# Performance work log

Hardware: AMD Instinct MI355X
Metric: run time of the kernel (lower is better)

The kernel has to match this reference:

```python
import jax, jax.numpy as jnp
import numpy as np

EPS = 1e-5

def _layernorm(x, g, b):
    mu = jnp.mean(x, axis=-1, keepdims=True)
    var = jnp.mean(jnp.square(x - mu), axis=-1, keepdims=True)
    return (x - mu) * jax.lax.rsqrt(var + EPS) * g + b

def setup_inputs() -> dict:
    key = jax.random.key(0)
    ks = jax.random.split(key, 5)
    dims, head = 1024, 16
    b, n = 2, 2048
    s = 0.02
    return {
        "x": jax.random.normal(ks[0], (b, n, dims), dtype=jnp.float32),
        "ln_g": jnp.ones((dims,), dtype=jnp.float32),
        "ln_b": jnp.zeros((dims,), dtype=jnp.float32),
        "W_kv": jax.random.normal(ks[1], (dims, 2 * dims), dtype=jnp.float32) * s,
        "W_x": jax.random.normal(ks[2], (head, head), dtype=jnp.float32) * s,
        "W_xa": jax.random.normal(ks[3], (head, head), dtype=jnp.float32) * s,
        "W_out": jax.random.normal(ks[4], (dims, dims), dtype=jnp.float32) * s,
    }

def reference(x, ln_g, ln_b, W_kv, W_x, W_xa, W_out):
    # attentiond.forward with xa=None, mask=None (self.que / self.rope are unused in the original forward)
    b, n, dims = x.shape
    head = W_x.shape[0]
    hd = dims // head
    h = _layernorm(x, ln_g, ln_b)
    kv = h @ W_kv                               # [b, n, 2*dims]
    qk, v = jnp.split(kv, 2, axis=-1)
    # xa is None -> qka = qk, va = v
    qk = qk.reshape(b, n, head, hd).transpose(0, 2, 1, 3)   # [b, h, n, d]
    v = v.reshape(b, n, head, hd).transpose(0, 2, 1, 3)
    scores = jnp.einsum('bhqd,bhkd->bhqk', qk, qk)          # full score matrix (no 1/sqrt(d) scale in original)
    a1 = jax.nn.softmax(scores, axis=-1)
    a2 = jax.nn.softmax(scores, axis=-2)
    # 1x1 Conv2d over head channel = head-mixing matmul: out[g] = sum_h W[g,h] * in[h]
    a1 = jnp.einsum('gh,bhqk->bgqk', W_x, a1)
    a2 = jnp.einsum('gh,bhqk->bgqk', W_xa, a2)
    o1 = jnp.einsum('bhij,bhjd->bhid', a1, v)               # used path (va == v)
    _o2 = jnp.einsum('bhji,bhjd->bhid', a2, v)              # computed in original but discarded (dead code)
    o1 = o1.transpose(0, 2, 1, 3).reshape(b, n, dims)
    return o1 @ W_out
```

## Files before the change

### kernel.cpp

```cpp
#include <hip/hip_runtime.h>
#include <math.h>

constexpr int Bb   = 2;
constexpr int Nn   = 2048;
constexpr int Dd   = 1024;
constexpr int Hh   = 16;
constexpr int HD   = 64;
constexpr int KVW  = 2*Dd;
constexpr int KSL  = 512;
constexpr float SHIFT = 20.f;

typedef short bf16x8 __attribute__((ext_vector_type(8)));
typedef float f32x4  __attribute__((ext_vector_type(4)));

__device__ inline float bf2f(unsigned short u){
  union { unsigned int i; float f; } x; x.i = ((unsigned int)u) << 16; return x.f;
}
__device__ inline unsigned short f2bf(float f){
  union { float f; unsigned int i; } x; x.f = f;
  unsigned int r = x.i + 0x7fffu + ((x.i >> 16) & 1u);
  return (unsigned short)(r >> 16);
}
__device__ inline void storeC(float* p, float v, int accum){ if (accum) *p += v; else *p = v; }
__device__ inline void storeC(unsigned short* p, float v, int){ *p = f2bf(v); }

__global__ __launch_bounds__(256) void ln_kernel(const float* __restrict__ x,
    const float* __restrict__ g, const float* __restrict__ bta, unsigned short* __restrict__ h){
  int row = blockIdx.x, tid = threadIdx.x;
  const float4* x4 = (const float4*)(x + (size_t)row*Dd);
  float4 v = x4[tid];
  float s  = v.x+v.y+v.z+v.w;
  float s2 = v.x*v.x+v.y*v.y+v.z*v.z+v.w*v.w;
#pragma unroll
  for (int off=32; off>0; off>>=1){ s += __shfl_down(s,off); s2 += __shfl_down(s2,off); }
  __shared__ float red[8];
  if ((tid&63)==0){ red[tid>>6]=s; red[4+(tid>>6)]=s2; }
  __syncthreads();
  s  = red[0]+red[1]+red[2]+red[3];
  s2 = red[4]+red[5]+red[6]+red[7];
  float mu = s*(1.f/Dd);
  float rs = rsqrtf(fmaxf(s2*(1.f/Dd)-mu*mu,0.f)+1e-5f);
  float4 gv=((const float4*)g)[tid], bv=((const float4*)bta)[tid];
  ushort4 o;
  o.x=f2bf((v.x-mu)*rs*gv.x+bv.x); o.y=f2bf((v.y-mu)*rs*gv.y+bv.y);
  o.z=f2bf((v.z-mu)*rs*gv.z+bv.z); o.w=f2bf((v.w-mu)*rs*gv.w+bv.w);
  ((ushort4*)(h+(size_t)row*Dd))[tid]=o;
}

__global__ __launch_bounds__(256) void wT_kernel(const float* __restrict__ in,
    unsigned short* __restrict__ out, int R, int Cc){
  __shared__ float t[32][33];
  int c0 = blockIdx.x*32, r0 = blockIdx.y*32;
  int tx = threadIdx.x&31, ty = threadIdx.x>>5;
#pragma unroll
  for (int k=0;k<4;k++)
    t[ty+8*k][tx] = in[(size_t)(r0+ty+8*k)*Cc + c0+tx];
  __syncthreads();
#pragma unroll
  for (int k=0;k<4;k++)
    out[(size_t)(c0+ty+8*k)*R + r0+tx] = f2bf(t[tx][ty+8*k]);
}

__global__ __launch_bounds__(256) void vT_kernel(const unsigned short* __restrict__ kvb,
    unsigned short* __restrict__ vT){
  __shared__ unsigned short t[32][33];
  int b = blockIdx.z;
  int d0 = blockIdx.x*32, k0 = blockIdx.y*32;
  const unsigned short* in = kvb + (size_t)b*Nn*KVW + Dd;
  unsigned short* out = vT + (size_t)b*Dd*Nn;
  int tx = threadIdx.x&31, ty = threadIdx.x>>5;
#pragma unroll
  for (int k=0;k<4;k++)
    t[ty+8*k][tx] = in[(size_t)(k0+ty+8*k)*KVW + d0+tx];
  __syncthreads();
#pragma unroll
  for (int k=0;k<4;k++)
    out[(size_t)(d0+ty+8*k)*Nn + k0+tx] = t[tx][ty+8*k];
}

__global__ __launch_bounds__(256) void cvt_kernel(const float* __restrict__ in,
    unsigned short* __restrict__ out){
  int i = blockIdx.x*256 + threadIdx.x;
  float4 v = ((const float4*)in)[i];
  ushort4 o; o.x=f2bf(v.x); o.y=f2bf(v.y); o.z=f2bf(v.z); o.w=f2bf(v.w);
  ((ushort4*)out)[i] = o;
}

__global__ __launch_bounds__(256) void zero_kernel(float* __restrict__ p){
  ((float4*)p)[blockIdx.x*256 + threadIdx.x] = float4{0.f,0.f,0.f,0.f};
}

template <int BN, typename CT>
__global__ __launch_bounds__(256) void mgemm(
    const unsigned short* __restrict__ A, const unsigned short* __restrict__ Bt,
    CT* __restrict__ C, int K, int lda, int ldb, int ldc,
    long sAz, long sBz, long sCz, int accum){
  constexpr int BM = 128, BK = 32;
  constexpr int RS = 40;
  constexpr int WC = (BN==128)?2:1;
  constexpr int WR = 4/WC;
  constexpr int FM = BM/(WR*16);
  constexpr int FN = BN/(WC*16);
  __shared__ __align__(16) short As[BM*RS];
  __shared__ __align__(16) short Bs[BN*RS];
  int tid = threadIdx.x;
  long z = blockIdx.z;
  const unsigned short* Ab = A + z*sAz + (size_t)blockIdx.y*BM*lda;
  const unsigned short* Bb = Bt + z*sBz + (size_t)blockIdx.x*BN*ldb;
  CT* Cb = C + z*sCz + (size_t)blockIdx.y*BM*ldc + (size_t)blockIdx.x*BN;
  int wid = tid>>6, lane = tid&63;
  int wr = (WC==2)?(wid>>1):wid;
  int wc = (WC==2)?(wid&1):0;
  int r0 = tid>>2, s0 = tid&3;
  f32x4 acc[FM][FN] = {};
  int nk = K/BK;
  uint4 a0, a1, b0, b1;
  a0 = *(const uint4*)(Ab + (size_t)r0*lda + s0*8);
  a1 = *(const uint4*)(Ab + (size_t)(r0+64)*lda + s0*8);
  b0 = *(const uint4*)(Bb + (size_t)r0*ldb + s0*8);
  if constexpr (BN==128) b1 = *(const uint4*)(Bb + (size_t)(r0+64)*ldb + s0*8);
  *(uint4*)&As[r0*RS + s0*8]      = a0;
  *(uint4*)&As[(r0+64)*RS + s0*8] = a1;
  *(uint4*)&Bs[r0*RS + s0*8]      = b0;
  if constexpr (BN==128) *(uint4*)&Bs[(r0+64)*RS + s0*8] = b1;
  __syncthreads();
  for (int t=0; t<nk; t++){
    if (t+1 < nk){
      int k0 = (t+1)*BK;
      a0 = *(const uint4*)(Ab + (size_t)r0*lda + k0 + s0*8);
      a1 = *(const uint4*)(Ab + (size_t)(r0+64)*lda + k0 + s0*8);
      b0 = *(const uint4*)(Bb + (size_t)r0*ldb + k0 + s0*8);
      if constexpr (BN==128) b1 = *(const uint4*)(Bb + (size_t)(r0+64)*ldb + k0 + s0*8);
    }
    bf16x8 af[FM], bfr[FN];
#pragma unroll
    for (int m=0;m<FM;m++){
      int row = wr*(FM*16) + m*16 + (lane&15);
      af[m] = *(const bf16x8*)&As[row*RS + (lane>>4)*8];
    }
#pragma unroll
    for (int n=0;n<FN;n++){
      int col = wc*(FN*16) + n*16 + (lane&15);
      bfr[n] = *(const bf16x8*)&Bs[col*RS + (lane>>4)*8];
    }
#pragma unroll
    for (int m=0;m<FM;m++)
#pragma unroll
      for (int n=0;n<FN;n++)
        acc[m][n] = __builtin_amdgcn_mfma_f32_16x16x32_bf16(af[m], bfr[n], acc[m][n], 0, 0, 0);
    if (t+1 < nk){
      __syncthreads();
      *(uint4*)&As[r0*RS + s0*8]      = a0;
      *(uint4*)&As[(r0+64)*RS + s0*8] = a1;
      *(uint4*)&Bs[r0*RS + s0*8]      = b0;
      if constexpr (BN==128) *(uint4*)&Bs[(r0+64)*RS + s0*8] = b1;
      __syncthreads();
    }
  }
#pragma unroll
  for (int m=0;m<FM;m++){
    int row = wr*(FM*16) + m*16 + (lane>>4)*4;
#pragma unroll
    for (int n=0;n<FN;n++){
      int col = wc*(FN*16) + n*16 + (lane&15);
#pragma unroll
      for (int rg=0;rg<4;rg++)
        storeC(Cb + (size_t)(row+rg)*ldc + col, acc[m][n][rg], accum);
    }
  }
}

__global__ __launch_bounds__(256) void sqexp_kernel(
    const unsigned short* __restrict__ A,
    const unsigned short* __restrict__ Bt,
    unsigned short* __restrict__ U,
    float* __restrict__ lsum){
  constexpr int BM = 128, BN = 128, BK = 32, RS = 40;
  constexpr int FM = 4, FN = 4;
  __shared__ __align__(16) short As[BM*RS];
  __shared__ __align__(16) short Bs[BN*RS];
  int tid = threadIdx.x;
  long z = blockIdx.z;
  const unsigned short* Ab = A + z*HD + (size_t)blockIdx.y*BM*KVW;
  const unsigned short* Bb = Bt + z*HD + (size_t)blockIdx.x*BN*KVW;
  unsigned short* Ub = U + z*(size_t)Nn*Nn + (size_t)blockIdx.y*BM*Nn + (size_t)blockIdx.x*BN;
  float* lrow = lsum + z*Nn + blockIdx.y*BM;
  int wid = tid>>6, lane = tid&63;
  int wr = wid>>1, wc = wid&1;
  int r0 = tid>>2, s0 = tid&3;
  f32x4 acc[FM][FN] = {};
  uint4 a0, a1, b0, b1;
  a0 = *(const uint4*)(Ab + (size_t)r0*KVW + s0*8);
  a1 = *(const uint4*)(Ab + (size_t)(r0+64)*KVW + s0*8);
  b0 = *(const uint4*)(Bb + (size_t)r0*KVW + s0*8);
  b1 = *(const uint4*)(Bb + (size_t)(r0+64)*KVW + s0*8);
  *(uint4*)&As[r0*RS + s0*8]      = a0;
  *(uint4*)&As[(r0+64)*RS + s0*8] = a1;
  *(uint4*)&Bs[r0*RS + s0*8]      = b0;
  *(uint4*)&Bs[(r0+64)*RS + s0*8] = b1;
  __syncthreads();
  for (int t=0; t<HD/BK; t++){
    if (t == 0){
      a0 = *(const uint4*)(Ab + (size_t)r0*KVW + BK + s0*8);
      a1 = *(const uint4*)(Ab + (size_t)(r0+64)*KVW + BK + s0*8);
      b0 = *(const uint4*)(Bb + (size_t)r0*KVW + BK + s0*8);
      b1 = *(const uint4*)(Bb + (size_t)(r0+64)*KVW + BK + s0*8);
    }
    bf16x8 af[FM], bfr[FN];
#pragma unroll
    for (int m=0;m<FM;m++)
      af[m] = *(const bf16x8*)&As[(wr*64 + m*16 + (lane&15))*RS + (lane>>4)*8];
#pragma unroll
    for (int n=0;n<FN;n++)
      bfr[n] = *(const bf16x8*)&Bs[(wc*64 + n*16 + (lane&15))*RS + (lane>>4)*8];
#pragma unroll
    for (int m=0;m<FM;m++)
#pragma unroll
      for (int n=0;n<FN;n++)
        acc[m][n] = __builtin_amdgcn_mfma_f32_16x16x32_bf16(af[m], bfr[n], acc[m][n], 0, 0, 0);
    if (t == 0){
      __syncthreads();
      *(uint4*)&As[r0*RS + s0*8]      = a0;
      *(uint4*)&As[(r0+64)*RS + s0*8] = a1;
      *(uint4*)&Bs[r0*RS + s0*8]      = b0;
      *(uint4*)&Bs[(r0+64)*RS + s0*8] = b1;
      __syncthreads();
    }
  }
  float part[FM][4];
#pragma unroll
  for (int m=0;m<FM;m++)
#pragma unroll
    for (int rg=0;rg<4;rg++) part[m][rg] = 0.f;
#pragma unroll
  for (int m=0;m<FM;m++){
    int row = wr*64 + m*16 + (lane>>4)*4;
#pragma unroll
    for (int n=0;n<FN;n++){
      int col = wc*64 + n*16 + (lane&15);
#pragma unroll
      for (int rg=0;rg<4;rg++){
        float e = __expf(acc[m][n][rg] - SHIFT);
        Ub[(size_t)(row+rg)*Nn + col] = f2bf(e);
        part[m][rg] += e;
      }
    }
  }
#pragma unroll
  for (int m=0;m<FM;m++)
#pragma unroll
    for (int rg=0;rg<4;rg++){
      float s = part[m][rg];
#pragma unroll
      for (int off=1; off<16; off<<=1) s += __shfl_xor(s, off);
      if ((lane&15)==0)
        atomicAdd(&lrow[wr*64 + m*16 + (lane>>4)*4 + rg], s);
    }
}

__global__ __launch_bounds__(256) void mix2s_kernel(
    const unsigned short* __restrict__ U, const float* __restrict__ Wx,
    const float* __restrict__ lsum, unsigned short* __restrict__ PM, int k0){
  int tid = threadIdx.x;
  int qr = tid>>7;
  int q  = blockIdx.x*2 + qr;
  int kk = (tid&127)*4;
  __shared__ float Wl[256];
  __shared__ float rl[2][16];
  Wl[tid] = Wx[tid];
  if (tid < 32) rl[tid>>4][tid&15] = 1.f/lsum[(size_t)(tid&15)*Nn + blockIdx.x*2 + (tid>>4)];
  __syncthreads();
  int ks = k0 + kk;
  float pm[16][4] = {};
#pragma unroll
  for (int h=0;h<16;h++){
    ushort4 u4 = *(const ushort4*)&U[((size_t)h*Nn+q)*Nn + ks];
    float r = rl[qr][h];
    float f0=bf2f(u4.x)*r, f1=bf2f(u4.y)*r, f2=bf2f(u4.z)*r, f3=bf2f(u4.w)*r;
#pragma unroll
    for (int g=0;g<16;g++){
      float w = Wl[g*16+h];
      pm[g][0]+=w*f0; pm[g][1]+=w*f1; pm[g][2]+=w*f2; pm[g][3]+=w*f3;
    }
  }
#pragma unroll
  for (int g=0;g<16;g++){
    ushort4 o;
    o.x=f2bf(pm[g][0]); o.y=f2bf(pm[g][1]); o.z=f2bf(pm[g][2]); o.w=f2bf(pm[g][3]);
    *(ushort4*)&PM[((size_t)g*Nn+q)*KSL + kk] = o;
  }
}

extern "C" void kernel_launch(void* const* d_in, const int* in_sizes, int n_in,
                              void* d_out, int out_size, void* d_ws, size_t ws_size,
                              hipStream_t stream){
  (void)in_sizes; (void)n_in; (void)out_size; (void)ws_size;
  const float* x    = (const float*)d_in[0];
  const float* lng  = (const float*)d_in[1];
  const float* lnb  = (const float*)d_in[2];
  const float* Wkv  = (const float*)d_in[3];
  const float* Wx   = (const float*)d_in[4];
  const float* Wout = (const float*)d_in[6];
  float* out = (float*)d_out;

  char* p = (char*)d_ws;
  unsigned short* h_b   = (unsigned short*)p;
  float*          o1    = (float*)p;
  p += (size_t)Bb*Nn*Dd*2;
  unsigned short* kvb   = (unsigned short*)p; p += (size_t)Bb*Nn*KVW*2;
  unsigned short* WkvT  = (unsigned short*)p; p += (size_t)KVW*Dd*2;
  unsigned short* WoutT = (unsigned short*)p; p += (size_t)Dd*Dd*2;
  unsigned short* vTb   = (unsigned short*)p; p += (size_t)Bb*Dd*Nn*2;
  unsigned short* o1b   = (unsigned short*)p; p += (size_t)Bb*Nn*Dd*2;
  float*          lb    = (float*)p;          p += (size_t)Bb*Hh*Nn*4;
  unsigned short* U     = (unsigned short*)p; p += (size_t)Hh*Nn*Nn*2;
  unsigned short* PM    = (unsigned short*)p;

  wT_kernel<<<dim3(KVW/32, Dd/32), 256, 0, stream>>>(Wkv, WkvT, Dd, KVW);
  wT_kernel<<<dim3(Dd/32, Dd/32), 256, 0, stream>>>(Wout, WoutT, Dd, Dd);
  ln_kernel<<<Bb*Nn, 256, 0, stream>>>(x, lng, lnb, h_b);
  mgemm<128, unsigned short><<<dim3(KVW/128, (Bb*Nn)/128, 1), 256, 0, stream>>>(
      h_b, WkvT, kvb, Dd, Dd, Dd, KVW, 0, 0, 0, 0);
  vT_kernel<<<dim3(Dd/32, Nn/32, Bb), 256, 0, stream>>>(kvb, vTb);
  zero_kernel<<<(Bb*Hh*Nn)/1024, 256, 0, stream>>>(lb);

  for (int b=0;b<Bb;b++){
    const unsigned short* kvb_b = kvb + (size_t)b*Nn*KVW;
    float* lb_b = lb + (size_t)b*Hh*Nn;
    sqexp_kernel<<<dim3(Nn/128, Nn/128, Hh), 256, 0, stream>>>(kvb_b, kvb_b, U, lb_b);
    for (int k0=0;k0<Nn;k0+=KSL){
      mix2s_kernel<<<Nn/2, 256, 0, stream>>>(U, Wx, lb_b, PM, k0);
      mgemm<64, float><<<dim3(1, Nn/128, Hh), 256, 0, stream>>>(
          PM, vTb + (size_t)b*Dd*Nn + k0, o1,
          KSL, KSL, Nn, Dd, (long)Nn*KSL, (long)64*Nn, 64, k0>0);
    }
    cvt_kernel<<<(Nn*Dd)/1024, 256, 0, stream>>>(o1, o1b + (size_t)b*Nn*Dd);
  }
  mgemm<128, float><<<dim3(Dd/128, (Bb*Nn)/128, 1), 256, 0, stream>>>(
      o1b, WoutT, out, Dd, Dd, Dd, Dd, 0, 0, 0, 0);
}
```

Before: 490.0 us.

## Recompute QK^T scores in fused exp-mix kernel instead of storing U

The old path wrote the exponentiated score tensor U to memory in bf16 and read it back in the mixing kernel. That path is replaced by a stats-only pass that computes row sums, plus a fused kernel that recomputes QK^T with MFMA, exponentiates, normalizes and mixes heads before writing PM. The K-slice loop, the float accumulation buffer and the conversion kernel are gone: the PV GEMM now runs over full K and writes bf16 output directly. The trade-off is computing the score GEMM twice to save a large write and read of the score tensor, with a full-size PM buffer in place of slices.

New measurement: 408.7 us. 16.6% less time.

```diff
diff --git a/kernel.cpp b/kernel.cpp
--- a/kernel.cpp
+++ b/kernel.cpp
@@ -7,7 +7,6 @@
 constexpr int Hh   = 16;
 constexpr int HD   = 64;
 constexpr int KVW  = 2*Dd;
-constexpr int KSL  = 512;
 constexpr float SHIFT = 20.f;
 
 typedef short bf16x8 __attribute__((ext_vector_type(8)));
@@ -76,14 +75,6 @@
 #pragma unroll
   for (int k=0;k<4;k++)
     out[(size_t)(d0+ty+8*k)*Nn + k0+tx] = t[tx][ty+8*k];
-}
-
-__global__ __launch_bounds__(256) void cvt_kernel(const float* __restrict__ in,
-    unsigned short* __restrict__ out){
-  int i = blockIdx.x*256 + threadIdx.x;
-  float4 v = ((const float4*)in)[i];
-  ushort4 o; o.x=f2bf(v.x); o.y=f2bf(v.y); o.z=f2bf(v.z); o.w=f2bf(v.w);
-  ((ushort4*)out)[i] = o;
 }
 
 __global__ __launch_bounds__(256) void zero_kernel(float* __restrict__ p){
@@ -170,21 +161,19 @@
   }
 }
 
-__global__ __launch_bounds__(256) void sqexp_kernel(
-    const unsigned short* __restrict__ A,
-    const unsigned short* __restrict__ Bt,
-    unsigned short* __restrict__ U,
+__global__ __launch_bounds__(256) void statsl_kernel(
+    const unsigned short* __restrict__ kvb,
     float* __restrict__ lsum){
-  constexpr int BM = 128, BN = 128, BK = 32, RS = 40;
+  constexpr int BK = 32, RS = 40;
   constexpr int FM = 4, FN = 4;
-  __shared__ __align__(16) short As[BM*RS];
-  __shared__ __align__(16) short Bs[BN*RS];
+  __shared__ __align__(16) short As[128*RS];
+  __shared__ __align__(16) short Bs[128*RS];
   int tid = threadIdx.x;
-  long z = blockIdx.z;
-  const unsigned short* Ab = A + z*HD + (size_t)blockIdx.y*BM*KVW;
-  const unsigned short* Bb = Bt + z*HD + (size_t)blockIdx.x*BN*KVW;
-  unsigned short* Ub = U + z*(size_t)Nn*Nn + (size_t)blockIdx.y*BM*Nn + (size_t)blockIdx.x*BN;
-  float* lrow = lsum + z*Nn + blockIdx.y*BM;
+  int z = blockIdx.z;
+  const unsigned short* base = kvb + (size_t)(z>>4)*Nn*KVW + (z&15)*HD;
+  const unsigned short* Ab = base + (size_t)blockIdx.y*128*KVW;
+  const unsigned short* Bq = base + (size_t)blockIdx.x*128*KVW;
+  float* lrow = lsum + (size_t)z*Nn + blockIdx.y*128;
   int wid = tid>>6, lane = tid&63;
   int wr = wid>>1, wc = wid&1;
   int r0 = tid>>2, s0 = tid&3;
@@ -192,8 +181,8 @@
   uint4 a0, a1, b0, b1;
   a0 = *(const uint4*)(Ab + (size_t)r0*KVW + s0*8);
   a1 = *(const uint4*)(Ab + (size_t)(r0+64)*KVW + s0*8);
-  b0 = *(const uint4*)(Bb + (size_t)r0*KVW + s0*8);
-  b1 = *(const uint4*)(Bb + (size_t)(r0+64)*KVW + s0*8);
+  b0 = *(const uint4*)(Bq + (size_t)r0*KVW + s0*8);
+  b1 = *(const uint4*)(Bq + (size_t)(r0+64)*KVW + s0*8);
   *(uint4*)&As[r0*RS + s0*8]      = a0;
   *(uint4*)&As[(r0+64)*RS + s0*8] = a1;
   *(uint4*)&Bs[r0*RS + s0*8]      = b0;
@@ -203,8 +192,8 @@
     if (t == 0){
       a0 = *(const uint4*)(Ab + (size_t)r0*KVW + BK + s0*8);
       a1 = *(const uint4*)(Ab + (size_t)(r0+64)*KVW + BK + s0*8);
-      b0 = *(const uint4*)(Bb + (size_t)r0*KVW + BK + s0*8);
-      b1 = *(const uint4*)(Bb + (size_t)(r0+64)*KVW + BK + s0*8);
+      b0 = *(const uint4*)(Bq + (size_t)r0*KVW + BK + s0*8);
+      b1 = *(const uint4*)(Bq + (size_t)(r0+64)*KVW + BK + s0*8);
     }
     bf16x8 af[FM], bfr[FN];
 #pragma unroll
@@ -233,19 +222,12 @@
 #pragma unroll
     for (int rg=0;rg<4;rg++) part[m][rg] = 0.f;
 #pragma unroll
-  for (int m=0;m<FM;m++){
-    int row = wr*64 + m*16 + (lane>>4)*4;
-#pragma unroll
-    for (int n=0;n<FN;n++){
-      int col = wc*64 + n*16 + (lane&15);
-#pragma unroll
-      for (int rg=0;rg<4;rg++){
-        float e = __expf(acc[m][n][rg] - SHIFT);
-        Ub[(size_t)(row+rg)*Nn + col] = f2bf(e);
-        part[m][rg] += e;
-      }
-    }
-  }
+  for (int m=0;m<FM;m++)
+#pragma unroll
+    for (int n=0;n<FN;n++)
+#pragma unroll
+      for (int rg=0;rg<4;rg++)
+        part[m][rg] += __expf(acc[m][n][rg] - SHIFT);
 #pragma unroll
   for (int m=0;m<FM;m++)
 #pragma unroll
@@ -258,36 +240,77 @@
     }
 }
 
-__global__ __launch_bounds__(256) void mix2s_kernel(
-    const unsigned short* __restrict__ U, const float* __restrict__ Wx,
-    const float* __restrict__ lsum, unsigned short* __restrict__ PM, int k0){
+__global__ __launch_bounds__(256) void mixexp_kernel(
+    const unsigned short* __restrict__ kvb_b,
+    const float* __restrict__ Wx,
+    const float* __restrict__ lsum_b,
+    unsigned short* __restrict__ PM){
+  constexpr int QS = 72;
+  __shared__ __align__(16) short Qs[16*QS];
+  __shared__ __align__(16) short Ks[64*QS];
+  __shared__ float Wl[256];
+  __shared__ float rls[16][16];
   int tid = threadIdx.x;
-  int qr = tid>>7;
-  int q  = blockIdx.x*2 + qr;
-  int kk = (tid&127)*4;
-  __shared__ float Wl[256];
-  __shared__ float rl[2][16];
+  int k0 = blockIdx.x*64, q0 = blockIdx.y*16;
+  int wv = tid>>6, lane = tid&63;
   Wl[tid] = Wx[tid];
-  if (tid < 32) rl[tid>>4][tid&15] = 1.f/lsum[(size_t)(tid&15)*Nn + blockIdx.x*2 + (tid>>4)];
-  __syncthreads();
-  int ks = k0 + kk;
-  float pm[16][4] = {};
-#pragma unroll
-  for (int h=0;h<16;h++){
-    ushort4 u4 = *(const ushort4*)&U[((size_t)h*Nn+q)*Nn + ks];
-    float r = rl[qr][h];
-    float f0=bf2f(u4.x)*r, f1=bf2f(u4.y)*r, f2=bf2f(u4.z)*r, f3=bf2f(u4.w)*r;
-#pragma unroll
-    for (int g=0;g<16;g++){
-      float w = Wl[g*16+h];
-      pm[g][0]+=w*f0; pm[g][1]+=w*f1; pm[g][2]+=w*f2; pm[g][3]+=w*f3;
-    }
-  }
-#pragma unroll
-  for (int g=0;g<16;g++){
-    ushort4 o;
-    o.x=f2bf(pm[g][0]); o.y=f2bf(pm[g][1]); o.z=f2bf(pm[g][2]); o.w=f2bf(pm[g][3]);
-    *(ushort4*)&PM[((size_t)g*Nn+q)*KSL + kk] = o;
+  {
+    int h = tid>>4, r = tid&15;
+    rls[h][r] = 1.f/lsum_b[(size_t)h*Nn + q0 + r];
+  }
+  int qr = tid>>4, qc = (tid&15)*4;
+  int kr = tid>>2, kc = (tid&3)*16;
+  const unsigned short* Qg = kvb_b + (size_t)(q0+qr)*KVW + qc;
+  const unsigned short* Kg = kvb_b + (size_t)(k0+kr)*KVW + kc;
+  uint2 qv; uint4 kv0, kv1;
+  qv  = *(const uint2*)(Qg);
+  kv0 = *(const uint4*)(Kg);
+  kv1 = *(const uint4*)(Kg + 8);
+  *(uint2*)&Qs[qr*QS + qc]     = qv;
+  *(uint4*)&Ks[kr*QS + kc]     = kv0;
+  *(uint4*)&Ks[kr*QS + kc + 8] = kv1;
+  __syncthreads();
+  float pmacc[16][4] = {};
+  for (int h=0; h<16; h++){
+    if (h+1 < 16){
+      qv  = *(const uint2*)(Qg + (h+1)*64);
+      kv0 = *(const uint4*)(Kg + (h+1)*64);
+      kv1 = *(const uint4*)(Kg + (h+1)*64 + 8);
+    }
+    bf16x8 af0 = *(const bf16x8*)&Qs[(lane&15)*QS + (lane>>4)*8];
+    bf16x8 af1 = *(const bf16x8*)&Qs[(lane&15)*QS + (lane>>4)*8 + 32];
+    bf16x8 bf0 = *(const bf16x8*)&Ks[(wv*16+(lane&15))*QS + (lane>>4)*8];
+    bf16x8 bf1 = *(const bf16x8*)&Ks[(wv*16+(lane&15))*QS + (lane>>4)*8 + 32];
+    f32x4 acc = {};
+    acc = __builtin_amdgcn_mfma_f32_16x16x32_bf16(af0, bf0, acc, 0, 0, 0);
+    acc = __builtin_amdgcn_mfma_f32_16x16x32_bf16(af1, bf1, acc, 0, 0, 0);
+    float er[4];
+#pragma unroll
+    for (int rg=0; rg<4; rg++)
+      er[rg] = __expf(acc[rg] - SHIFT) * rls[h][(lane>>4)*4 + rg];
+#pragma unroll
+    for (int g=0; g<16; g++){
+      float w = Wl[g*16 + h];
+#pragma unroll
+      for (int rg=0; rg<4; rg++) pmacc[g][rg] += w*er[rg];
+    }
+    if (h+1 < 16){
+      __syncthreads();
+      *(uint2*)&Qs[qr*QS + qc]     = qv;
+      *(uint4*)&Ks[kr*QS + kc]     = kv0;
+      *(uint4*)&Ks[kr*QS + kc + 8] = kv1;
+      __syncthreads();
+    }
+  }
+  int col = k0 + wv*16 + (lane&15);
+#pragma unroll
+  for (int g=0; g<16; g++){
+    unsigned short* Pg = PM + ((size_t)g*Nn + q0)*Nn + col;
+#pragma unroll
+    for (int rg=0; rg<4; rg++){
+      int row = (lane>>4)*4 + rg;
+      Pg[(size_t)row*Nn] = f2bf(pmacc[g][rg]);
+    }
   }
 }
 
@@ -304,16 +327,13 @@
   float* out = (float*)d_out;
 
   char* p = (char*)d_ws;
-  unsigned short* h_b   = (unsigned short*)p;
-  float*          o1    = (float*)p;
-  p += (size_t)Bb*Nn*Dd*2;
+  unsigned short* h_b   = (unsigned short*)p; p += (size_t)Bb*Nn*Dd*2;
   unsigned short* kvb   = (unsigned short*)p; p += (size_t)Bb*Nn*KVW*2;
   unsigned short* WkvT  = (unsigned short*)p; p += (size_t)KVW*Dd*2;
   unsigned short* WoutT = (unsigned short*)p; p += (size_t)Dd*Dd*2;
   unsigned short* vTb   = (unsigned short*)p; p += (size_t)Bb*Dd*Nn*2;
   unsigned short* o1b   = (unsigned short*)p; p += (size_t)Bb*Nn*Dd*2;
   float*          lb    = (float*)p;          p += (size_t)Bb*Hh*Nn*4;
-  unsigned short* U     = (unsigned short*)p; p += (size_t)Hh*Nn*Nn*2;
   unsigned short* PM    = (unsigned short*)p;
 
   wT_kernel<<<dim3(KVW/32, Dd/32), 256, 0, stream>>>(Wkv, WkvT, Dd, KVW);
@@ -324,17 +344,15 @@
   vT_kernel<<<dim3(Dd/32, Nn/32, Bb), 256, 0, stream>>>(kvb, vTb);
   zero_kernel<<<(Bb*Hh*Nn)/1024, 256, 0, stream>>>(lb);
 
+  statsl_kernel<<<dim3(Nn/128, Nn/128, Bb*Hh), 256, 0, stream>>>(kvb, lb);
+
   for (int b=0;b<Bb;b++){
     const unsigned short* kvb_b = kvb + (size_t)b*Nn*KVW;
-    float* lb_b = lb + (size_t)b*Hh*Nn;
-    sqexp_kernel<<<dim3(Nn/128, Nn/128, Hh), 256, 0, stream>>>(kvb_b, kvb_b, U, lb_b);
-    for (int k0=0;k0<Nn;k0+=KSL){
-      mix2s_kernel<<<Nn/2, 256, 0, stream>>>(U, Wx, lb_b, PM, k0);
-      mgemm<64, float><<<dim3(1, Nn/128, Hh), 256, 0, stream>>>(
-          PM, vTb + (size_t)b*Dd*Nn + k0, o1,
-          KSL, KSL, Nn, Dd, (long)Nn*KSL, (long)64*Nn, 64, k0>0);
-    }
-    cvt_kernel<<<(Nn*Dd)/1024, 256, 0, stream>>>(o1, o1b + (size_t)b*Nn*Dd);
+    const float* lb_b = lb + (size_t)b*Hh*Nn;
+    mixexp_kernel<<<dim3(Nn/64, Nn/16), 256, 0, stream>>>(kvb_b, Wx, lb_b, PM);
+    mgemm<64, unsigned short><<<dim3(1, Nn/128, Hh), 256, 0, stream>>>(
+        PM, vTb + (size_t)b*Dd*Nn, o1b + (size_t)b*Nn*Dd,
+        Nn, Nn, Nn, Dd, (long)Nn*Nn, (long)64*Nn, 64, 0);
   }
   mgemm<128, float><<<dim3(Dd/128, (Bb*Nn)/128, 1), 256, 0, stream>>>(
       o1b, WoutT, out, Dd, Dd, Dd, Dd, 0, 0, 0, 0);
```
